# Kernel tuning notes

Hardware: AMD Instinct MI355X
Metric: run time of the kernel (lower is better)

Reference implementation:

```python
import jax, jax.numpy as jnp
import numpy as np

B, S, D, H = 2, 2048, 1024, 16
HD = D // H  # head dim = 64


def setup_inputs() -> dict:
    key = jax.random.key(0)
    ks = jax.random.split(key, 9)
    s = 1.0 / np.sqrt(D)
    return {
        "hidden_states": jax.random.normal(ks[0], (B, S, D), dtype=jnp.float32),
        "attention_mask": jnp.zeros((B, 1, 1, S), dtype=jnp.float32),
        "Wq": jax.random.normal(ks[1], (D, D), dtype=jnp.float32) * s,
        "bq": jnp.zeros((D,), dtype=jnp.float32),
        "Wk": jax.random.normal(ks[2], (D, D), dtype=jnp.float32) * s,
        "bk": jnp.zeros((D,), dtype=jnp.float32),
        "Wv": jax.random.normal(ks[3], (D, D), dtype=jnp.float32) * s,
        "bv": jnp.zeros((D,), dtype=jnp.float32),
        "Wo": jax.random.normal(ks[4], (D, D), dtype=jnp.float32) * s,
        "bo": jnp.zeros((D,), dtype=jnp.float32),
    }


def reference(hidden_states, attention_mask, Wq, bq, Wk, bk, Wv, bv, Wo, bo):
    b, s = hidden_states.shape[:2]
    # QKV projections -> [b, h, s, hd]
    def proj(W, bias):
        y = hidden_states @ W.T + bias
        return y.reshape(b, s, H, HD).transpose(0, 2, 1, 3)
    q = proj(Wq, bq)
    k = proj(Wk, bk)
    v = proj(Wv, bv)
    scores = jnp.einsum("bhqd,bhkd->bhqk", q, k) / jnp.sqrt(jnp.float32(HD))
    scores = scores + attention_mask  # additive mask, broadcast [b,1,1,s]
    probs = jax.nn.softmax(scores, axis=-1)  # dropout p=0 (eval)
    ctx = jnp.einsum("bhqk,bhkd->bhqd", probs, v)
    ctx = ctx.transpose(0, 2, 1, 3).reshape(b, s, D)
    out = ctx @ Wo.T + bo
    return (out, probs)
```

## Files before the change

kernel.cpp:

```cpp
#include <hip/hip_runtime.h>
#include <hip/hip_bf16.h>

#define B_ 2
#define S_ 2048
#define D_ 1024
#define H_ 16
#define HD_ 64

typedef short bf16x8 __attribute__((ext_vector_type(8)));
typedef float f32x4 __attribute__((ext_vector_type(4)));

typedef __attribute__((address_space(3))) void lds_void;
typedef const __attribute__((address_space(1))) void gbl_void;

__device__ __forceinline__ f32x4 mfma16(bf16x8 a, bf16x8 b, f32x4 c) {
    return __builtin_amdgcn_mfma_f32_16x16x32_bf16(a, b, c, 0, 0, 0);
}

__device__ __forceinline__ bf16x8 ldb8(const __hip_bfloat16* p) {
    return *reinterpret_cast<const bf16x8*>(p);
}

__global__ __launch_bounds__(256) void conv_all(
    const float* __restrict__ hs, const float* __restrict__ Wq,
    const float* __restrict__ Wk, const float* __restrict__ Wv,
    const float* __restrict__ Wo,
    __hip_bfloat16* __restrict__ hsb, __hip_bfloat16* __restrict__ wqkvb,
    __hip_bfloat16* __restrict__ wob) {
    const int i = blockIdx.x * 256 + threadIdx.x;
    const float* src;
    __hip_bfloat16* dst;
    int off;
    if (i < (1 << 20)) {
        src = hs; dst = hsb; off = i;
    } else {
        const int j = i - (1 << 20);
        const int r = j >> 18;
        off = j & 0x3ffff;
        src = (r == 0) ? Wq : (r == 1) ? Wk : (r == 2) ? Wv : Wo;
        dst = (r < 3) ? wqkvb + (size_t)r * 1048576 : wob;
    }
    float4 f = reinterpret_cast<const float4*>(src)[off];
    union { __hip_bfloat16 h[4]; ushort4 u; } cv;
    cv.h[0] = __float2bfloat16(f.x);
    cv.h[1] = __float2bfloat16(f.y);
    cv.h[2] = __float2bfloat16(f.z);
    cv.h[3] = __float2bfloat16(f.w);
    reinterpret_cast<ushort4*>(dst)[off] = cv.u;
}

template <int MODE>
__global__ __launch_bounds__(256) void gemm_bt(
    const __hip_bfloat16* __restrict__ X, const __hip_bfloat16* __restrict__ Wt,
    const float* __restrict__ bias0, const float* __restrict__ bias1,
    const float* __restrict__ bias2,
    __hip_bfloat16* __restrict__ Yq, __hip_bfloat16* __restrict__ Yk,
    __hip_bfloat16* __restrict__ Yv, float* __restrict__ Yo,
    int M, int N, int K) {
    __shared__ __hip_bfloat16 As[128 * 32];
    __shared__ __hip_bfloat16 Bs[128 * 32];

    const int ntn = N >> 7;
    const int nwg = (M >> 7) * ntn;
    const int cpx = nwg >> 3;
    const int bid = blockIdx.x;
    const int lg = (bid & 7) * cpx + (bid >> 3);
    const int tm = lg / ntn;
    const int tn = lg % ntn;
    const int t = threadIdx.x;
    const int w = t >> 6, l = t & 63, g = l >> 4, c = l & 15;
    const int wr = w >> 1, wc = w & 1;

    const int lrow16 = l >> 2;
    const int lcol = (l & 3) * 8;

    const int r0 = w * 32 + lrow16;
    const int r1 = w * 32 + 16 + lrow16;
    const size_t xg0 = (size_t)(tm * 128 + r0) * K + lcol;
    const size_t xg1 = (size_t)(tm * 128 + r1) * K + lcol;
    const size_t wg0 = (size_t)(tn * 128 + r0) * K + lcol;
    const size_t wg1 = (size_t)(tn * 128 + r1) * K + lcol;

    f32x4 acc[4][4] = {};

    for (int k0 = 0; k0 < K; k0 += 32) {
        __syncthreads();
        __builtin_amdgcn_global_load_lds((gbl_void*)(X + xg0 + k0),
                                         (lds_void*)(As + (w * 32) * 32), 16, 0, 0);
        __builtin_amdgcn_global_load_lds((gbl_void*)(X + xg1 + k0),
                                         (lds_void*)(As + (w * 32 + 16) * 32), 16, 0, 0);
        __builtin_amdgcn_global_load_lds((gbl_void*)(Wt + wg0 + k0),
                                         (lds_void*)(Bs + (w * 32) * 32), 16, 0, 0);
        __builtin_amdgcn_global_load_lds((gbl_void*)(Wt + wg1 + k0),
                                         (lds_void*)(Bs + (w * 32 + 16) * 32), 16, 0, 0);
        __syncthreads();

        bf16x8 am[4], bn[4];
#pragma unroll
        for (int mi = 0; mi < 4; ++mi) am[mi] = ldb8(&As[(wr * 64 + mi * 16 + c) * 32 + g * 8]);
#pragma unroll
        for (int ni = 0; ni < 4; ++ni) bn[ni] = ldb8(&Bs[(wc * 64 + ni * 16 + c) * 32 + g * 8]);
#pragma unroll
        for (int mi = 0; mi < 4; ++mi)
#pragma unroll
            for (int ni = 0; ni < 4; ++ni)
                acc[mi][ni] = mfma16(am[mi], bn[ni], acc[mi][ni]);
    }

#pragma unroll
    for (int mi = 0; mi < 4; ++mi) {
        const int mbase = tm * 128 + wr * 64 + mi * 16 + g * 4;
#pragma unroll
        for (int ni = 0; ni < 4; ++ni) {
            const int n = tn * 128 + wc * 64 + ni * 16 + c;
            if (MODE == 0) {
                const float* bp = (n < 1024) ? bias0 : (n < 2048) ? bias1 : bias2;
                const int nn = n & 1023;
                const float bias = bp[nn];
                const int h = nn >> 6, hd = nn & 63;
                const int b = mbase >> 11, s0 = mbase & 2047;
                const size_t bh = (size_t)(b * H_ + h);
                if (n < 2048) {
                    __hip_bfloat16* dst = (n < 1024) ? Yq : Yk;
#pragma unroll
                    for (int r = 0; r < 4; ++r)
                        dst[(bh * S_ + s0 + r) * HD_ + hd] =
                            __float2bfloat16(acc[mi][ni][r] + bias);
                } else {
                    union { __hip_bfloat16 hh[4]; ushort4 u4; } pk;
#pragma unroll
                    for (int r = 0; r < 4; ++r)
                        pk.hh[r] = __float2bfloat16(acc[mi][ni][r] + bias);
                    *reinterpret_cast<ushort4*>(&Yv[(bh * HD_ + hd) * S_ + s0]) = pk.u4;
                }
            } else {
#pragma unroll
                for (int r = 0; r < 4; ++r)
                    Yo[(size_t)(mbase + r) * N + n] = acc[mi][ni][r] + bias0[n];
            }
        }
    }
}

#define STAGE_K(dstc, t8v) do {                                                   \
    const int kt_ = (t8v) * 256;                                                  \
    _Pragma("unroll")                                                             \
    for (int i_ = 0; i_ < 4; ++i_) {                                              \
        const int chunk_ = w * 4 + i_;                                            \
        const int row_ = 8 * chunk_ + (l >> 3);                                   \
        const int col_ = ((l & 7) ^ ((l >> 3) & 7)) * 8;                          \
        __builtin_amdgcn_global_load_lds(                                         \
            (gbl_void*)(Kb + (size_t)(kt_ + row_) * HD_ + col_),                  \
            (lds_void*)((dstc) + chunk_ * 1024), 16, 0, 0);                       \
    }                                                                             \
} while (0)

#define STAGE_VP(dstc, t8v) do {                                                  \
    const int kb_ = ((t8v) * 256 + 32 * w) * 2;                                   \
    _Pragma("unroll")                                                             \
    for (int i_ = 0; i_ < 4; ++i_) {                                              \
        const int row_ = 16 * i_ + (l >> 2);                                      \
        const int scol_ = ((l & 3) * 16) ^ ((row_ & 3) << 4);                     \
        __builtin_amdgcn_global_load_lds(                                         \
            (gbl_void*)((const char*)Vb + (size_t)row_ * (S_ * 2) + kb_ + scol_), \
            (lds_void*)((dstc) + w * 4096 + i_ * 1024), 16, 0, 0);                \
    }                                                                             \
} while (0)

__global__ __launch_bounds__(512, 4) void attn_kernel(
    const __hip_bfloat16* __restrict__ Qh, const __hip_bfloat16* __restrict__ Kh,
    const __hip_bfloat16* __restrict__ Vt, const float* __restrict__ mask,
    float* __restrict__ probs, __hip_bfloat16* __restrict__ ctx) {
    union SMem {
        char KV[2][32768];
        float Cred[8][16][68];
    };
    __shared__ SMem sm;
    __shared__ float msk[2048];
    __shared__ float sred[8][16];
    __shared__ float invsh[16];

    const int bid = blockIdx.x;
    const int lg = (bid & 7) * 512 + (bid >> 3);
    const int qt = lg & 127;
    const int bh = lg >> 7;
    const int b = bh >> 4, h = bh & 15;
    const int t = threadIdx.x;
    const int w = t >> 6, l = t & 63, g = l >> 4, c = l & 15;
    const int q0 = qt * 16;
    const int kw = 32 * w;

    const __hip_bfloat16* Qb = Qh + (size_t)bh * S_ * HD_;
    const __hip_bfloat16* Kb = Kh + (size_t)bh * S_ * HD_;
    const __hip_bfloat16* Vb = Vt + (size_t)bh * HD_ * S_;
    const float* mrow = mask + (size_t)b * S_;

    *reinterpret_cast<float4*>(&msk[t * 4]) =
        *reinterpret_cast<const float4*>(&mrow[t * 4]);

    const bf16x8 aq0 = ldb8(&Qb[(q0 + c) * HD_ + g * 8]);
    const bf16x8 aq1 = ldb8(&Qb[(q0 + c) * HD_ + 32 + g * 8]);

    __syncthreads();

    unsigned int uA[8][2][2];
    float lsum = 0.f;

    STAGE_K(sm.KV[0], 0);
#pragma unroll
    for (int t8 = 0; t8 < 8; ++t8) {
        const char* cur = sm.KV[t8 & 1];
        if (t8 < 7) {
            STAGE_K(sm.KV[(t8 & 1) ^ 1], t8 + 1);
            asm volatile("s_waitcnt vmcnt(4)" ::: "memory");
        } else {
            asm volatile("s_waitcnt vmcnt(0)" ::: "memory");
        }
        __builtin_amdgcn_sched_barrier(0);
        const int kt = t8 * 256;
#pragma unroll
        for (int ss = 0; ss < 2; ++ss) {
            const int krow = kw + ss * 16 + c;
            const char* kb2 = cur + krow * 128;
            const int sw = (krow & 7) << 4;
            const bf16x8 k0 = *reinterpret_cast<const bf16x8*>(kb2 + ((g * 16) ^ sw));
            const bf16x8 k1 = *reinterpret_cast<const bf16x8*>(kb2 + ((64 + g * 16) ^ sw));
            f32x4 aA = {};
            aA = mfma16(k0, aq0, aA);
            aA = mfma16(k1, aq1, aA);
            const float4 mk = *reinterpret_cast<const float4*>(&msk[kt + kw + ss * 16 + g * 4]);
            const float p0 = __expf(aA[0] * 0.125f + mk.x);
            const float p1 = __expf(aA[1] * 0.125f + mk.y);
            const float p2 = __expf(aA[2] * 0.125f + mk.z);
            const float p3 = __expf(aA[3] * 0.125f + mk.w);
            lsum += (p0 + p1) + (p2 + p3);
            union { __hip_bfloat16 hh[2]; unsigned int ui; } w0, w1;
            w0.hh[0] = __float2bfloat16(p0); w0.hh[1] = __float2bfloat16(p1);
            w1.hh[0] = __float2bfloat16(p2); w1.hh[1] = __float2bfloat16(p3);
            uA[t8][ss][0] = w0.ui; uA[t8][ss][1] = w1.ui;
        }
        __builtin_amdgcn_sched_barrier(0);
    }

    lsum += __shfl_xor(lsum, 16);
    lsum += __shfl_xor(lsum, 32);
    if (g == 0) sred[w][c] = lsum;
    asm volatile("s_waitcnt lgkmcnt(0)" ::: "memory");
    __builtin_amdgcn_s_barrier();
    __builtin_amdgcn_sched_barrier(0);
    float tot = 0.f;
#pragma unroll
    for (int w8 = 0; w8 < 8; ++w8) tot += sred[w8][c];
    const float invA = 1.0f / tot;
    if (w == 0 && g == 0) invsh[c] = invA;

    f32x4 cacc[4] = {};
    float* prowA = probs + ((size_t)bh * S_ + q0 + c) * S_;
    const int src0 = 32 * (g & 1) + c;
    const int src1 = src0 + 16;
    const int sigma = g >> 1;
    STAGE_VP(sm.KV[0], 0);
#pragma unroll
    for (int t8 = 0; t8 < 8; ++t8) {
        const char* curV = sm.KV[t8 & 1] + w * 4096;
        if (t8 < 7) STAGE_VP(sm.KV[(t8 & 1) ^ 1], t8 + 1);
        if (t8 == 0)      asm volatile("s_waitcnt vmcnt(4)" ::: "memory");
        else if (t8 == 7) asm volatile("s_waitcnt vmcnt(2)" ::: "memory");
        else              asm volatile("s_waitcnt vmcnt(6)" ::: "memory");
        __builtin_amdgcn_sched_barrier(0);
        const int kt = t8 * 256;
#pragma unroll
        for (int ss = 0; ss < 2; ++ss) {
            f32x4 oA;
            oA[0] = __uint_as_float(uA[t8][ss][0] << 16) * invA;
            oA[1] = __uint_as_float(uA[t8][ss][0] & 0xffff0000u) * invA;
            oA[2] = __uint_as_float(uA[t8][ss][1] << 16) * invA;
            oA[3] = __uint_as_float(uA[t8][ss][1] & 0xffff0000u) * invA;
            *reinterpret_cast<f32x4*>(&prowA[kt + kw + ss * 16 + g * 4]) = oA;
        }
        union { unsigned int ui[4]; bf16x8 v; } afA;
        {
            const unsigned int x00 = __shfl(uA[t8][0][0], src0);
            const unsigned int x10 = __shfl(uA[t8][1][0], src0);
            const unsigned int x01 = __shfl(uA[t8][0][1], src0);
            const unsigned int x11 = __shfl(uA[t8][1][1], src0);
            const unsigned int x02 = __shfl(uA[t8][0][0], src1);
            const unsigned int x12 = __shfl(uA[t8][1][0], src1);
            const unsigned int x03 = __shfl(uA[t8][0][1], src1);
            const unsigned int x13 = __shfl(uA[t8][1][1], src1);
            afA.ui[0] = sigma ? x10 : x00;
            afA.ui[1] = sigma ? x11 : x01;
            afA.ui[2] = sigma ? x12 : x02;
            afA.ui[3] = sigma ? x13 : x03;
        }
#pragma unroll
        for (int n = 0; n < 4; ++n) {
            const int vrow = n * 16 + c;
            const bf16x8 bv = *reinterpret_cast<const bf16x8*>(
                curV + vrow * 64 + ((g * 16) ^ ((vrow & 3) << 4)));
            cacc[n] = mfma16(afA.v, bv, cacc[n]);
        }
        __builtin_amdgcn_sched_barrier(0);
    }

    __syncthreads();
#pragma unroll
    for (int n = 0; n < 4; ++n)
#pragma unroll
        for (int r = 0; r < 4; ++r)
            sm.Cred[w][g * 4 + r][n * 16 + c] = cacc[n][r];
    __syncthreads();
    {
        const int row = t >> 5, col2 = (t & 31) * 2;
        float a0 = 0.f, a1 = 0.f;
#pragma unroll
        for (int w8 = 0; w8 < 8; ++w8) {
            const float2 vv = *reinterpret_cast<const float2*>(&sm.Cred[w8][row][col2]);
            a0 += vv.x; a1 += vv.y;
        }
        const float fin = invsh[row];
        union { __hip_bfloat16 hh[2]; unsigned int ui; } ov;
        ov.hh[0] = __float2bfloat16(a0 * fin);
        ov.hh[1] = __float2bfloat16(a1 * fin);
        *reinterpret_cast<unsigned int*>(
            &ctx[((size_t)b * S_ + q0 + row) * D_ + h * HD_ + col2]) = ov.ui;
    }
}

extern "C" void kernel_launch(void* const* d_in, const int* in_sizes, int n_in,
                              void* d_out, int out_size, void* d_ws, size_t ws_size,
                              hipStream_t stream) {
    const float* hs   = (const float*)d_in[0];
    const float* mask = (const float*)d_in[1];
    const float* Wq   = (const float*)d_in[2];
    const float* bq   = (const float*)d_in[3];
    const float* Wk   = (const float*)d_in[4];
    const float* bk   = (const float*)d_in[5];
    const float* Wv   = (const float*)d_in[6];
    const float* bv   = (const float*)d_in[7];
    const float* Wo   = (const float*)d_in[8];
    const float* bo   = (const float*)d_in[9];

    float* out   = (float*)d_out;
    float* probs = out + (size_t)B_ * S_ * D_;

    const size_t MD = (size_t)B_ * S_ * D_;
    __hip_bfloat16* hsb   = (__hip_bfloat16*)d_ws;
    __hip_bfloat16* wqkvb = hsb + MD;
    __hip_bfloat16* wob   = wqkvb + 3u * 1024u * 1024u;
    __hip_bfloat16* Qh    = wob + (size_t)1024 * 1024;
    __hip_bfloat16* Kh    = Qh + MD;
    __hip_bfloat16* Vt    = Kh + MD;
    __hip_bfloat16* ctxb  = Vt + MD;

    conv_all<<<8192, 256, 0, stream>>>(hs, Wq, Wk, Wv, Wo, hsb, wqkvb, wob);

    gemm_bt<0><<<32 * 24, 256, 0, stream>>>(hsb, wqkvb, bq, bk, bv,
                                            Qh, Kh, Vt, nullptr, 4096, 3072, 1024);

    attn_kernel<<<B_ * H_ * (S_ / 16), 512, 0, stream>>>(Qh, Kh, Vt, mask, probs, ctxb);

    gemm_bt<1><<<32 * 8, 256, 0, stream>>>(ctxb, wob, bo, nullptr, nullptr,
                                           nullptr, nullptr, nullptr, out, 4096, 1024, 1024);
}
```

Baseline: 272.9 us.

## Widen GEMM K-tile to 64 with XOR-swizzled LDS and transpose Q output

Result: faster. 265.8 us, median of 2 (-2.6%).

```diff
diff --git a/kernel.cpp b/kernel.cpp
--- a/kernel.cpp
+++ b/kernel.cpp
@@ -57,8 +57,8 @@
     __hip_bfloat16* __restrict__ Yq, __hip_bfloat16* __restrict__ Yk,
     __hip_bfloat16* __restrict__ Yv, float* __restrict__ Yo,
     int M, int N, int K) {
-    __shared__ __hip_bfloat16 As[128 * 32];
-    __shared__ __hip_bfloat16 Bs[128 * 32];
+    __shared__ __hip_bfloat16 As[128 * 64];
+    __shared__ __hip_bfloat16 Bs[128 * 64];
 
     const int ntn = N >> 7;
     const int nwg = (M >> 7) * ntn;
@@ -71,40 +71,49 @@
     const int w = t >> 6, l = t & 63, g = l >> 4, c = l & 15;
     const int wr = w >> 1, wc = w & 1;
 
-    const int lrow16 = l >> 2;
-    const int lcol = (l & 3) * 8;
-
-    const int r0 = w * 32 + lrow16;
-    const int r1 = w * 32 + 16 + lrow16;
-    const size_t xg0 = (size_t)(tm * 128 + r0) * K + lcol;
-    const size_t xg1 = (size_t)(tm * 128 + r1) * K + lcol;
-    const size_t wg0 = (size_t)(tn * 128 + r0) * K + lcol;
-    const size_t wg1 = (size_t)(tn * 128 + r1) * K + lcol;
+    const int srow = t >> 3;
+    const int schunk = t & 7;
 
     f32x4 acc[4][4] = {};
 
-    for (int k0 = 0; k0 < K; k0 += 32) {
+    for (int k0 = 0; k0 < K; k0 += 64) {
         __syncthreads();
-        __builtin_amdgcn_global_load_lds((gbl_void*)(X + xg0 + k0),
-                                         (lds_void*)(As + (w * 32) * 32), 16, 0, 0);
-        __builtin_amdgcn_global_load_lds((gbl_void*)(X + xg1 + k0),
-                                         (lds_void*)(As + (w * 32 + 16) * 32), 16, 0, 0);
-        __builtin_amdgcn_global_load_lds((gbl_void*)(Wt + wg0 + k0),
-                                         (lds_void*)(Bs + (w * 32) * 32), 16, 0, 0);
-        __builtin_amdgcn_global_load_lds((gbl_void*)(Wt + wg1 + k0),
-                                         (lds_void*)(Bs + (w * 32 + 16) * 32), 16, 0, 0);
+#pragma unroll
+        for (int j = 0; j < 4; ++j) {
+            const int row = j * 32 + srow;
+            const int se = (schunk ^ (row & 7)) * 8;
+            __builtin_amdgcn_global_load_lds(
+                (gbl_void*)(X + (size_t)(tm * 128 + row) * K + k0 + se),
+                (lds_void*)(As + (j * 32 + w * 8) * 64), 16, 0, 0);
+            __builtin_amdgcn_global_load_lds(
+                (gbl_void*)(Wt + (size_t)(tn * 128 + row) * K + k0 + se),
+                (lds_void*)(Bs + (j * 32 + w * 8) * 64), 16, 0, 0);
+        }
         __syncthreads();
 
-        bf16x8 am[4], bn[4];
-#pragma unroll
-        for (int mi = 0; mi < 4; ++mi) am[mi] = ldb8(&As[(wr * 64 + mi * 16 + c) * 32 + g * 8]);
-#pragma unroll
-        for (int ni = 0; ni < 4; ++ni) bn[ni] = ldb8(&Bs[(wc * 64 + ni * 16 + c) * 32 + g * 8]);
-#pragma unroll
-        for (int mi = 0; mi < 4; ++mi)
-#pragma unroll
-            for (int ni = 0; ni < 4; ++ni)
-                acc[mi][ni] = mfma16(am[mi], bn[ni], acc[mi][ni]);
+#pragma unroll
+        for (int kh = 0; kh < 2; ++kh) {
+            bf16x8 am[4], bn[4];
+#pragma unroll
+            for (int mi = 0; mi < 4; ++mi) {
+                const int row = wr * 64 + mi * 16 + c;
+                am[mi] = *reinterpret_cast<const bf16x8*>(
+                    reinterpret_cast<const char*>(As) + row * 128 +
+                    ((kh * 64 + g * 16) ^ ((row & 7) << 4)));
+            }
+#pragma unroll
+            for (int ni = 0; ni < 4; ++ni) {
+                const int row = wc * 64 + ni * 16 + c;
+                bn[ni] = *reinterpret_cast<const bf16x8*>(
+                    reinterpret_cast<const char*>(Bs) + row * 128 +
+                    ((kh * 64 + g * 16) ^ ((row & 7) << 4)));
+            }
+#pragma unroll
+            for (int mi = 0; mi < 4; ++mi)
+#pragma unroll
+                for (int ni = 0; ni < 4; ++ni)
+                    acc[mi][ni] = mfma16(am[mi], bn[ni], acc[mi][ni]);
+        }
     }
 
 #pragma unroll
@@ -120,18 +129,18 @@
                 const int h = nn >> 6, hd = nn & 63;
                 const int b = mbase >> 11, s0 = mbase & 2047;
                 const size_t bh = (size_t)(b * H_ + h);
-                if (n < 2048) {
-                    __hip_bfloat16* dst = (n < 1024) ? Yq : Yk;
-#pragma unroll
-                    for (int r = 0; r < 4; ++r)
-                        dst[(bh * S_ + s0 + r) * HD_ + hd] =
-                            __float2bfloat16(acc[mi][ni][r] + bias);
-                } else {
+                if (n < 1024 || n >= 2048) {
+                    __hip_bfloat16* dst = (n < 1024) ? Yq : Yv;
                     union { __hip_bfloat16 hh[4]; ushort4 u4; } pk;
 #pragma unroll
                     for (int r = 0; r < 4; ++r)
                         pk.hh[r] = __float2bfloat16(acc[mi][ni][r] + bias);
-                    *reinterpret_cast<ushort4*>(&Yv[(bh * HD_ + hd) * S_ + s0]) = pk.u4;
+                    *reinterpret_cast<ushort4*>(&dst[(bh * HD_ + hd) * S_ + s0]) = pk.u4;
+                } else {
+#pragma unroll
+                    for (int r = 0; r < 4; ++r)
+                        Yk[(bh * S_ + s0 + r) * HD_ + hd] =
+                            __float2bfloat16(acc[mi][ni][r] + bias);
                 }
             } else {
 #pragma unroll
@@ -168,7 +177,7 @@
 } while (0)
 
 __global__ __launch_bounds__(512, 4) void attn_kernel(
-    const __hip_bfloat16* __restrict__ Qh, const __hip_bfloat16* __restrict__ Kh,
+    const __hip_bfloat16* __restrict__ Qt, const __hip_bfloat16* __restrict__ Kh,
     const __hip_bfloat16* __restrict__ Vt, const float* __restrict__ mask,
     float* __restrict__ probs, __hip_bfloat16* __restrict__ ctx) {
     union SMem {
@@ -190,7 +199,7 @@
     const int q0 = qt * 16;
     const int kw = 32 * w;
 
-    const __hip_bfloat16* Qb = Qh + (size_t)bh * S_ * HD_;
+    const __hip_bfloat16* Qb = Qt + (size_t)bh * HD_ * S_;
     const __hip_bfloat16* Kb = Kh + (size_t)bh * S_ * HD_;
     const __hip_bfloat16* Vb = Vt + (size_t)bh * HD_ * S_;
     const float* mrow = mask + (size_t)b * S_;
@@ -198,8 +207,14 @@
     *reinterpret_cast<float4*>(&msk[t * 4]) =
         *reinterpret_cast<const float4*>(&mrow[t * 4]);
 
-    const bf16x8 aq0 = ldb8(&Qb[(q0 + c) * HD_ + g * 8]);
-    const bf16x8 aq1 = ldb8(&Qb[(q0 + c) * HD_ + 32 + g * 8]);
+    union { ushort us[8]; bf16x8 v; } q0u, q1u;
+#pragma unroll
+    for (int e = 0; e < 8; ++e) {
+        q0u.us[e] = *reinterpret_cast<const ushort*>(&Qb[(size_t)(8 * g + e) * S_ + q0 + c]);
+        q1u.us[e] = *reinterpret_cast<const ushort*>(&Qb[(size_t)(32 + 8 * g + e) * S_ + q0 + c]);
+    }
+    const bf16x8 aq0 = q0u.v;
+    const bf16x8 aq1 = q1u.v;
 
     __syncthreads();
 
@@ -348,17 +363,17 @@
     __hip_bfloat16* hsb   = (__hip_bfloat16*)d_ws;
     __hip_bfloat16* wqkvb = hsb + MD;
     __hip_bfloat16* wob   = wqkvb + 3u * 1024u * 1024u;
-    __hip_bfloat16* Qh    = wob + (size_t)1024 * 1024;
-    __hip_bfloat16* Kh    = Qh + MD;
+    __hip_bfloat16* Qtb   = wob + (size_t)1024 * 1024;
+    __hip_bfloat16* Kh    = Qtb + MD;
     __hip_bfloat16* Vt    = Kh + MD;
     __hip_bfloat16* ctxb  = Vt + MD;
 
     conv_all<<<8192, 256, 0, stream>>>(hs, Wq, Wk, Wv, Wo, hsb, wqkvb, wob);
 
     gemm_bt<0><<<32 * 24, 256, 0, stream>>>(hsb, wqkvb, bq, bk, bv,
-                                            Qh, Kh, Vt, nullptr, 4096, 3072, 1024);
-
-    attn_kernel<<<B_ * H_ * (S_ / 16), 512, 0, stream>>>(Qh, Kh, Vt, mask, probs, ctxb);
+                                            Qtb, Kh, Vt, nullptr, 4096, 3072, 1024);
+
+    attn_kernel<<<B_ * H_ * (S_ / 16), 512, 0, stream>>>(Qtb, Kh, Vt, mask, probs, ctxb);
 
     gemm_bt<1><<<32 * 8, 256, 0, stream>>>(ctxb, wob, bo, nullptr, nullptr,
                                            nullptr, nullptr, nullptr, out, 4096, 1024, 1024);
```
